# Optimization experiments

Measured on AMD Instinct MI355X. Metric: run time of the kernel, lower is better.

## Reference

```python
import jax, jax.numpy as jnp
import numpy as np

IN_C = 256
OUT_C = 256
HID = IN_C * 2
N_POINTS = 262144
N_NODES = 8192
B = 16
MAX_NODES = 512
EPS = 1e-5


def _mlp(h, w1, b1, g1, be1, w2, b2):
    # PyG MLP([C, 2C, out], norm='layer_norm'): lin -> layernorm -> relu -> (dropout, eval=identity) -> lin
    h = h @ w1 + b1
    mu = jnp.mean(h, axis=-1, keepdims=True)
    var = jnp.var(h, axis=-1, keepdims=True)
    h = (h - mu) * jax.lax.rsqrt(var + EPS) * g1 + be1
    h = jax.nn.relu(h)
    return h @ w2 + b2


def setup_inputs() -> dict:
    key = jax.random.key(0)
    ks = jax.random.split(key, 16)
    x = jax.random.normal(ks[0], (N_POINTS, IN_C), dtype=jnp.float32)
    f_point_batches = jnp.sort(jax.random.randint(ks[1], (N_POINTS,), 0, N_NODES)).astype(jnp.int32)
    # equal-sized graphs (16 graphs x 512 nodes), sorted as torch.split/pad_sequence assume
    g_node_batches = jnp.repeat(jnp.arange(B, dtype=jnp.int32), MAX_NODES)
    s = 1.0 / np.sqrt(IN_C)
    s2 = 1.0 / np.sqrt(HID)
    def lin(k, fan_in, shape, scale):
        return jax.random.uniform(k, shape, jnp.float32, -scale, scale)
    params = {}
    for i, name in enumerate(['Wq', 'Wk']):
        base = 2 + i * 6
        params[f'{name}_w1'] = lin(ks[base + 0], IN_C, (IN_C, HID), s)
        params[f'{name}_b1'] = lin(ks[base + 1], IN_C, (HID,), s)
        params[f'{name}_g1'] = jnp.ones((HID,), jnp.float32)
        params[f'{name}_be1'] = jnp.zeros((HID,), jnp.float32)
        params[f'{name}_w2'] = lin(ks[base + 2], HID, (HID, OUT_C), s2)
        params[f'{name}_b2'] = lin(ks[base + 3], HID, (OUT_C,), s2)
    return dict(x=x, f_point_batches=f_point_batches, g_node_batches=g_node_batches,
                num_graphs=B, max_nodes=MAX_NODES, **params)


def reference(x, f_point_batches, g_node_batches, num_graphs, max_nodes,
              Wq_w1, Wq_b1, Wq_g1, Wq_be1, Wq_w2, Wq_b2,
              Wk_w1, Wk_b1, Wk_g1, Wk_be1, Wk_w2, Wk_b2):
    n_nodes = g_node_batches.shape[0]
    C = x.shape[1]
    # scatter_mean over points -> per-node feature means [n_nodes, C]
    sums = jax.ops.segment_sum(x, f_point_batches, num_segments=n_nodes)
    cnt = jax.ops.segment_sum(jnp.ones((x.shape[0],), x.dtype), f_point_batches, num_segments=n_nodes)
    mean = sums / jnp.maximum(cnt, 1.0)[:, None]
    # ragged split by graph + pad_sequence -> [B, max_nodes, C]
    starts = jnp.searchsorted(g_node_batches, jnp.arange(num_graphs, dtype=g_node_batches.dtype))
    pos = jnp.arange(n_nodes) - starts[g_node_batches]
    padded = jnp.zeros((num_graphs, max_nodes, C), x.dtype).at[g_node_batches, pos].set(mean, mode='drop')
    q = _mlp(padded, Wq_w1, Wq_b1, Wq_g1, Wq_be1, Wq_w2, Wq_b2)  # [B, MAXN, out]
    k = _mlp(padded, Wk_w1, Wk_b1, Wk_g1, Wk_be1, Wk_w2, Wk_b2)
    return jnp.einsum('bnd,bmd->bnm', q, k)  # bmm(q, k^T)
```

## Files before the change

### kernel.cpp

```cpp
#include <hip/hip_runtime.h>
#include <hip/hip_bf16.h>

#define N_POINTS 262144
#define N_NODES  8192
#define IN_C     256
#define HID      512
#define OUT_C    256
#define NB       16
#define MAXN     512
#define EPSV     1e-5f
#define NPB      32

typedef __attribute__((ext_vector_type(8))) short short8;
typedef __attribute__((ext_vector_type(4))) float f32x4;
typedef __attribute__((ext_vector_type(4))) float f4v;
#define MFMA16(a, b, c) __builtin_amdgcn_mfma_f32_16x16x32_bf16((a), (b), (c), 0, 0, 0)


__global__ __launch_bounds__(256) void prelude_k(
    const int* __restrict__ fpb, int* __restrict__ starts,
    const float* __restrict__ W1q, const float* __restrict__ W1k,
    const float* __restrict__ W2q, const float* __restrict__ W2k,
    __hip_bfloat16* __restrict__ P1q, __hip_bfloat16* __restrict__ P1k,
    __hip_bfloat16* __restrict__ P2q, __hip_bfloat16* __restrict__ P2k)
{
  if (blockIdx.x < 1024) {
    const int i = blockIdx.x * 256 + threadIdx.x;
    const int cur = fpb[i];
    const int prev = (i == 0) ? -1 : fpb[i - 1];
    for (int n = prev + 1; n <= cur; ++n) starts[n] = i;
    if (i == N_POINTS - 1)
      for (int n = cur + 1; n <= N_NODES; ++n) starts[n] = N_POINTS;
    return;
  }
  const int bid = blockIdx.x - 1024;
  const int sel = bid >> 6;
  const float* W; __hip_bfloat16* P; int N;
  switch (sel) {
    case 0:  W = W1q; P = P1q; N = HID;   break;
    case 1:  W = W1k; P = P1k; N = HID;   break;
    case 2:  W = W2q; P = P2q; N = OUT_C; break;
    default: W = W2k; P = P2k; N = OUT_C; break;
  }
  const int idx = (bid & 63) * 256 + threadIdx.x;
  const int NF = N >> 4;
  const int lane = idx & 63;
  const int nf = (idx >> 6) % NF;
  const int ks = idx / (64 * NF);
  const int k0 = ks * 32 + (lane >> 4) * 8;
  const int n  = nf * 16 + (lane & 15);
  __hip_bfloat16 tmp[8];
  #pragma unroll
  for (int j = 0; j < 8; ++j) tmp[j] = __float2bfloat16(W[(size_t)(k0 + j) * N + n]);
  *(uint4*)(P + (size_t)idx * 8) = *(uint4*)tmp;
}

__device__ __forceinline__ void accum_rows(
    const float* __restrict__ x, int lo, int hi, int l,
    f4v& a0, f4v& a1, f4v& a2, f4v& a3)
{
  int r = lo;
  for (; r + 4 <= hi; r += 4) {
    f4v v0 = *(const f4v*)(x + (size_t)(r + 0) * IN_C + l * 4);
    f4v v1 = *(const f4v*)(x + (size_t)(r + 1) * IN_C + l * 4);
    f4v v2 = *(const f4v*)(x + (size_t)(r + 2) * IN_C + l * 4);
    f4v v3 = *(const f4v*)(x + (size_t)(r + 3) * IN_C + l * 4);
    a0 += v0; a1 += v1; a2 += v2; a3 += v3;
  }
  for (; r < hi; ++r)
    a0 += *(const f4v*)(x + (size_t)r * IN_C + l * 4);
}

__global__ __launch_bounds__(512, 4) void fused_mlp_k(
    const float* __restrict__ x, const int* __restrict__ starts,
    const __hip_bfloat16* __restrict__ P1q, const __hip_bfloat16* __restrict__ P2q,
    const float* __restrict__ b1q, const float* __restrict__ g1q,
    const float* __restrict__ be1q, const float* __restrict__ b2q,
    const __hip_bfloat16* __restrict__ P1k, const __hip_bfloat16* __restrict__ P2k,
    const float* __restrict__ b1k, const float* __restrict__ g1k,
    const float* __restrict__ be1k, const float* __restrict__ b2k,
    __hip_bfloat16* __restrict__ qo, __hip_bfloat16* __restrict__ ko)
{
  const int n0 = blockIdx.x * NPB;
  const int t = threadIdx.x;
  const int w = t >> 6, l = t & 63, lg = l >> 4, lm = l & 15;

  __shared__ __hip_bfloat16 As[NPB * 264];
  __shared__ __hip_bfloat16 Hs[NPB * 520];
  __shared__ float lnp[8][NPB][2];

  #pragma unroll
  for (int i = 0; i < 4; ++i) {
    const int nl = w * 4 + i;
    const int node = n0 + nl;
    const int s_ = starts[node], e_ = starts[node + 1];
    f4v a0 = (f4v)0.f, a1 = (f4v)0.f, a2 = (f4v)0.f, a3 = (f4v)0.f;
    accum_rows(x, s_, e_, l, a0, a1, a2, a3);
    a0 += a1 + a2 + a3;
    const int cnt = e_ - s_;
    const float inv = cnt > 0 ? 1.0f / (float)cnt : 0.0f;
    __hip_bfloat16 o[4];
    o[0] = __float2bfloat16(a0.x * inv);
    o[1] = __float2bfloat16(a0.y * inv);
    o[2] = __float2bfloat16(a0.z * inv);
    o[3] = __float2bfloat16(a0.w * inv);
    *(uint2*)(As + nl * 264 + l * 4) = *(uint2*)o;
  }
  __syncthreads();

  for (int hh = 0; hh < 2; ++hh) {
    const __hip_bfloat16* P1 = hh ? P1k : P1q;
    const __hip_bfloat16* P2 = hh ? P2k : P2q;
    const float* b1  = hh ? b1k  : b1q;
    const float* g1  = hh ? g1k  : g1q;
    const float* be1 = hh ? be1k : be1q;
    const float* b2  = hh ? b2k  : b2q;
    __hip_bfloat16* out = hh ? ko : qo;

    f32x4 acc1[2][4];
    #pragma unroll
    for (int mi = 0; mi < 2; ++mi)
      #pragma unroll
      for (int nj = 0; nj < 4; ++nj)
        #pragma unroll
        for (int r = 0; r < 4; ++r) acc1[mi][nj][r] = 0.f;

    for (int ks = 0; ks < 8; ++ks) {
      short8 a0 = *(const short8*)(As + lm * 264 + ks * 32 + lg * 8);
      short8 a1 = *(const short8*)(As + (16 + lm) * 264 + ks * 32 + lg * 8);
      const __hip_bfloat16* bp = P1 + ((size_t)(ks * 32 + w * 4) * 64 + l) * 8;
      #pragma unroll
      for (int nj = 0; nj < 4; ++nj) {
        short8 b = *(const short8*)(bp + (size_t)nj * 512);
        acc1[0][nj] = MFMA16(a0, b, acc1[0][nj]);
        acc1[1][nj] = MFMA16(a1, b, acc1[1][nj]);
      }
    }

    float b1v[4], g1v[4], e1v[4];
    #pragma unroll
    for (int nj = 0; nj < 4; ++nj) {
      const int col = w * 64 + nj * 16 + lm;
      b1v[nj] = b1[col]; g1v[nj] = g1[col]; e1v[nj] = be1[col];
    }
    #pragma unroll
    for (int mi = 0; mi < 2; ++mi)
      #pragma unroll
      for (int nj = 0; nj < 4; ++nj)
        #pragma unroll
        for (int r = 0; r < 4; ++r) acc1[mi][nj][r] += b1v[nj];

    #pragma unroll
    for (int mi = 0; mi < 2; ++mi)
      #pragma unroll
      for (int r = 0; r < 4; ++r) {
        float s = 0.f, q = 0.f;
        #pragma unroll
        for (int nj = 0; nj < 4; ++nj) {
          const float v = acc1[mi][nj][r];
          s += v; q += v * v;
        }
        #pragma unroll
        for (int off = 1; off < 16; off <<= 1) {
          s += __shfl_xor(s, off);
          q += __shfl_xor(q, off);
        }
        if (lm == 0) {
          const int row = mi * 16 + lg * 4 + r;
          lnp[w][row][0] = s;
          lnp[w][row][1] = q;
        }
      }
    __syncthreads();

    #pragma unroll
    for (int mi = 0; mi < 2; ++mi)
      #pragma unroll
      for (int r = 0; r < 4; ++r) {
        const int row = mi * 16 + lg * 4 + r;
        float S = 0.f, Q = 0.f;
        #pragma unroll
        for (int w2 = 0; w2 < 8; ++w2) {
          S += lnp[w2][row][0];
          Q += lnp[w2][row][1];
        }
        const float mu = S * (1.0f / HID);
        const float rs = rsqrtf(Q * (1.0f / HID) - mu * mu + EPSV);
        #pragma unroll
        for (int nj = 0; nj < 4; ++nj) {
          const float y = (acc1[mi][nj][r] - mu) * rs * g1v[nj] + e1v[nj];
          Hs[row * 520 + w * 64 + nj * 16 + lm] = __float2bfloat16(fmaxf(y, 0.f));
        }
      }
    __syncthreads();

    f32x4 acc2[2][2];
    #pragma unroll
    for (int mi = 0; mi < 2; ++mi)
      #pragma unroll
      for (int nj = 0; nj < 2; ++nj)
        #pragma unroll
        for (int r = 0; r < 4; ++r) acc2[mi][nj][r] = 0.f;

    for (int ks = 0; ks < 16; ++ks) {
      short8 a0 = *(const short8*)(Hs + lm * 520 + ks * 32 + lg * 8);
      short8 a1 = *(const short8*)(Hs + (16 + lm) * 520 + ks * 32 + lg * 8);
      const __hip_bfloat16* bp = P2 + ((size_t)(ks * 16 + w * 2) * 64 + l) * 8;
      #pragma unroll
      for (int nj = 0; nj < 2; ++nj) {
        short8 b = *(const short8*)(bp + (size_t)nj * 512);
        acc2[0][nj] = MFMA16(a0, b, acc2[0][nj]);
        acc2[1][nj] = MFMA16(a1, b, acc2[1][nj]);
      }
    }

    float b2v[2];
    #pragma unroll
    for (int nj = 0; nj < 2; ++nj) b2v[nj] = b2[w * 32 + nj * 16 + lm];
    #pragma unroll
    for (int mi = 0; mi < 2; ++mi)
      #pragma unroll
      for (int nj = 0; nj < 2; ++nj)
        #pragma unroll
        for (int r = 0; r < 4; ++r) {
          const int row = n0 + mi * 16 + lg * 4 + r;
          const int col = w * 32 + nj * 16 + lm;
          out[(size_t)row * OUT_C + col] = __float2bfloat16(acc2[mi][nj][r] + b2v[nj]);
        }
    __syncthreads();
  }
}

__global__ __launch_bounds__(256, 4) void bmm_k(
    const __hip_bfloat16* __restrict__ q, const __hip_bfloat16* __restrict__ k,
    float* __restrict__ out)
{
  const int b  = blockIdx.z;
  const int n0 = blockIdx.x * 64;
  const int m0 = blockIdx.y * 64;
  const int t = threadIdx.x;
  const int w = t >> 6, l = t & 63, lg = l >> 4, lm = l & 15;

  const __hip_bfloat16* qb = q + ((size_t)b * MAXN + n0 + w * 16) * OUT_C;
  const __hip_bfloat16* kb = k + ((size_t)b * MAXN + m0) * OUT_C;

  f32x4 acc[4];
  #pragma unroll
  for (int nj = 0; nj < 4; ++nj)
    #pragma unroll
    for (int r = 0; r < 4; ++r) acc[nj][r] = 0.f;

  for (int ks = 0; ks < 8; ++ks) {
    short8 a = *(const short8*)(qb + (size_t)lm * OUT_C + ks * 32 + lg * 8);
    #pragma unroll
    for (int nj = 0; nj < 4; ++nj) {
      short8 bb = *(const short8*)(kb + (size_t)(nj * 16 + lm) * OUT_C + ks * 32 + lg * 8);
      acc[nj] = MFMA16(a, bb, acc[nj]);
    }
  }

  #pragma unroll
  for (int nj = 0; nj < 4; ++nj)
    #pragma unroll
    for (int r = 0; r < 4; ++r) {
      const int nrow = n0 + w * 16 + lg * 4 + r;
      const int mcol = m0 + nj * 16 + lm;
      out[((size_t)b * MAXN + nrow) * MAXN + mcol] = acc[nj][r];
    }
}

extern "C" void kernel_launch(void* const* d_in, const int* in_sizes, int n_in,
                              void* d_out, int out_size, void* d_ws, size_t ws_size,
                              hipStream_t stream)
{
  const float* x   = (const float*)d_in[0];
  const int*   fpb = (const int*)d_in[1];
  const float* Wq_w1  = (const float*)d_in[5];
  const float* Wq_b1  = (const float*)d_in[6];
  const float* Wq_g1  = (const float*)d_in[7];
  const float* Wq_be1 = (const float*)d_in[8];
  const float* Wq_w2  = (const float*)d_in[9];
  const float* Wq_b2  = (const float*)d_in[10];
  const float* Wk_w1  = (const float*)d_in[11];
  const float* Wk_b1  = (const float*)d_in[12];
  const float* Wk_g1  = (const float*)d_in[13];
  const float* Wk_be1 = (const float*)d_in[14];
  const float* Wk_w2  = (const float*)d_in[15];
  const float* Wk_b2  = (const float*)d_in[16];

  __hip_bfloat16* ws = (__hip_bfloat16*)d_ws;
  __hip_bfloat16* P1q  = ws;
  __hip_bfloat16* P1k  = P1q + 131072;
  __hip_bfloat16* P2q  = P1k + 131072;
  __hip_bfloat16* P2k  = P2q + 131072;
  __hip_bfloat16* qo   = P2k + 131072;
  __hip_bfloat16* ko   = qo + 2097152;
  int* starts = (int*)(ko + 2097152);
  float* out = (float*)d_out;

  prelude_k<<<1280, 256, 0, stream>>>(fpb, starts,
      Wq_w1, Wk_w1, Wq_w2, Wk_w2, P1q, P1k, P2q, P2k);
  fused_mlp_k<<<N_NODES / NPB, 512, 0, stream>>>(
      x, starts, P1q, P2q, Wq_b1, Wq_g1, Wq_be1, Wq_b2,
      P1k, P2k, Wk_b1, Wk_g1, Wk_be1, Wk_b2, qo, ko);
  bmm_k<<<dim3(8, 8, NB), 256, 0, stream>>>(qo, ko, out);
}
```

Before: 96.19 us.

## Run Q and K MLP heads concurrently with 1024-thread blocks

The fused MLP kernel doubles its block to 16 waves. The first 8 waves compute the Q head and the other 8 compute the K head at the same time, instead of looping over the two heads one after the other. Each wave now gathers scatter-mean for 2 nodes instead of 4. The hidden buffer and the layernorm partials are duplicated per head, which raises LDS use and per-block register pressure. Launch bounds of 1024 threads with 4 blocks requested may not be achievable, so occupancy could drop.

```diff
diff --git a/kernel.cpp b/kernel.cpp
--- a/kernel.cpp
+++ b/kernel.cpp
@@ -71,7 +71,7 @@
     a0 += *(const f4v*)(x + (size_t)r * IN_C + l * 4);
 }
 
-__global__ __launch_bounds__(512, 4) void fused_mlp_k(
+__global__ __launch_bounds__(1024, 4) void fused_mlp_k(
     const float* __restrict__ x, const int* __restrict__ starts,
     const __hip_bfloat16* __restrict__ P1q, const __hip_bfloat16* __restrict__ P2q,
     const float* __restrict__ b1q, const float* __restrict__ g1q,
@@ -84,14 +84,25 @@
   const int n0 = blockIdx.x * NPB;
   const int t = threadIdx.x;
   const int w = t >> 6, l = t & 63, lg = l >> 4, lm = l & 15;
+  const int h = w >> 3;
+  const int c = w & 7;
+
+  const __hip_bfloat16* P1 = h ? P1k : P1q;
+  const __hip_bfloat16* P2 = h ? P2k : P2q;
+  const float* b1  = h ? b1k  : b1q;
+  const float* g1  = h ? g1k  : g1q;
+  const float* be1 = h ? be1k : be1q;
+  const float* b2  = h ? b2k  : b2q;
+  __hip_bfloat16* out = h ? ko : qo;
 
   __shared__ __hip_bfloat16 As[NPB * 264];
-  __shared__ __hip_bfloat16 Hs[NPB * 520];
-  __shared__ float lnp[8][NPB][2];
-
-  #pragma unroll
-  for (int i = 0; i < 4; ++i) {
-    const int nl = w * 4 + i;
+  __shared__ __hip_bfloat16 Hs[2][NPB * 520];
+  __shared__ float lnp[16][NPB][2];
+  __hip_bfloat16* Hsh = Hs[h];
+
+  #pragma unroll
+  for (int i = 0; i < 2; ++i) {
+    const int nl = w * 2 + i;
     const int node = n0 + nl;
     const int s_ = starts[node], e_ = starts[node + 1];
     f4v a0 = (f4v)0.f, a1 = (f4v)0.f, a2 = (f4v)0.f, a3 = (f4v)0.f;
@@ -108,127 +119,116 @@
   }
   __syncthreads();
 
-  for (int hh = 0; hh < 2; ++hh) {
-    const __hip_bfloat16* P1 = hh ? P1k : P1q;
-    const __hip_bfloat16* P2 = hh ? P2k : P2q;
-    const float* b1  = hh ? b1k  : b1q;
-    const float* g1  = hh ? g1k  : g1q;
-    const float* be1 = hh ? be1k : be1q;
-    const float* b2  = hh ? b2k  : b2q;
-    __hip_bfloat16* out = hh ? ko : qo;
-
-    f32x4 acc1[2][4];
-    #pragma unroll
-    for (int mi = 0; mi < 2; ++mi)
-      #pragma unroll
-      for (int nj = 0; nj < 4; ++nj)
-        #pragma unroll
-        for (int r = 0; r < 4; ++r) acc1[mi][nj][r] = 0.f;
-
-    for (int ks = 0; ks < 8; ++ks) {
-      short8 a0 = *(const short8*)(As + lm * 264 + ks * 32 + lg * 8);
-      short8 a1 = *(const short8*)(As + (16 + lm) * 264 + ks * 32 + lg * 8);
-      const __hip_bfloat16* bp = P1 + ((size_t)(ks * 32 + w * 4) * 64 + l) * 8;
+  f32x4 acc1[2][4];
+  #pragma unroll
+  for (int mi = 0; mi < 2; ++mi)
+    #pragma unroll
+    for (int nj = 0; nj < 4; ++nj)
+      #pragma unroll
+      for (int r = 0; r < 4; ++r) acc1[mi][nj][r] = 0.f;
+
+  for (int ks = 0; ks < 8; ++ks) {
+    short8 a0 = *(const short8*)(As + lm * 264 + ks * 32 + lg * 8);
+    short8 a1 = *(const short8*)(As + (16 + lm) * 264 + ks * 32 + lg * 8);
+    const __hip_bfloat16* bp = P1 + ((size_t)(ks * 32 + c * 4) * 64 + l) * 8;
+    #pragma unroll
+    for (int nj = 0; nj < 4; ++nj) {
+      short8 b = *(const short8*)(bp + (size_t)nj * 512);
+      acc1[0][nj] = MFMA16(a0, b, acc1[0][nj]);
+      acc1[1][nj] = MFMA16(a1, b, acc1[1][nj]);
+    }
+  }
+
+  float b1v[4], g1v[4], e1v[4];
+  #pragma unroll
+  for (int nj = 0; nj < 4; ++nj) {
+    const int col = c * 64 + nj * 16 + lm;
+    b1v[nj] = b1[col]; g1v[nj] = g1[col]; e1v[nj] = be1[col];
+  }
+  #pragma unroll
+  for (int mi = 0; mi < 2; ++mi)
+    #pragma unroll
+    for (int nj = 0; nj < 4; ++nj)
+      #pragma unroll
+      for (int r = 0; r < 4; ++r) acc1[mi][nj][r] += b1v[nj];
+
+  #pragma unroll
+  for (int mi = 0; mi < 2; ++mi)
+    #pragma unroll
+    for (int r = 0; r < 4; ++r) {
+      float s = 0.f, q = 0.f;
       #pragma unroll
       for (int nj = 0; nj < 4; ++nj) {
-        short8 b = *(const short8*)(bp + (size_t)nj * 512);
-        acc1[0][nj] = MFMA16(a0, b, acc1[0][nj]);
-        acc1[1][nj] = MFMA16(a1, b, acc1[1][nj]);
-      }
-    }
-
-    float b1v[4], g1v[4], e1v[4];
-    #pragma unroll
-    for (int nj = 0; nj < 4; ++nj) {
-      const int col = w * 64 + nj * 16 + lm;
-      b1v[nj] = b1[col]; g1v[nj] = g1[col]; e1v[nj] = be1[col];
-    }
-    #pragma unroll
-    for (int mi = 0; mi < 2; ++mi)
-      #pragma unroll
-      for (int nj = 0; nj < 4; ++nj)
-        #pragma unroll
-        for (int r = 0; r < 4; ++r) acc1[mi][nj][r] += b1v[nj];
-
-    #pragma unroll
-    for (int mi = 0; mi < 2; ++mi)
+        const float v = acc1[mi][nj][r];
+        s += v; q += v * v;
+      }
+      #pragma unroll
+      for (int off = 1; off < 16; off <<= 1) {
+        s += __shfl_xor(s, off);
+        q += __shfl_xor(q, off);
+      }
+      if (lm == 0) {
+        const int row = mi * 16 + lg * 4 + r;
+        lnp[w][row][0] = s;
+        lnp[w][row][1] = q;
+      }
+    }
+  __syncthreads();
+
+  #pragma unroll
+  for (int mi = 0; mi < 2; ++mi)
+    #pragma unroll
+    for (int r = 0; r < 4; ++r) {
+      const int row = mi * 16 + lg * 4 + r;
+      float S = 0.f, Q = 0.f;
+      #pragma unroll
+      for (int w2 = 0; w2 < 8; ++w2) {
+        S += lnp[h * 8 + w2][row][0];
+        Q += lnp[h * 8 + w2][row][1];
+      }
+      const float mu = S * (1.0f / HID);
+      const float rs = rsqrtf(Q * (1.0f / HID) - mu * mu + EPSV);
+      #pragma unroll
+      for (int nj = 0; nj < 4; ++nj) {
+        const float y = (acc1[mi][nj][r] - mu) * rs * g1v[nj] + e1v[nj];
+        Hsh[row * 520 + c * 64 + nj * 16 + lm] = __float2bfloat16(fmaxf(y, 0.f));
+      }
+    }
+  __syncthreads();
+
+  f32x4 acc2[2][2];
+  #pragma unroll
+  for (int mi = 0; mi < 2; ++mi)
+    #pragma unroll
+    for (int nj = 0; nj < 2; ++nj)
+      #pragma unroll
+      for (int r = 0; r < 4; ++r) acc2[mi][nj][r] = 0.f;
+
+  for (int ks = 0; ks < 16; ++ks) {
+    short8 a0 = *(const short8*)(Hsh + lm * 520 + ks * 32 + lg * 8);
+    short8 a1 = *(const short8*)(Hsh + (16 + lm) * 520 + ks * 32 + lg * 8);
+    const __hip_bfloat16* bp = P2 + ((size_t)(ks * 16 + c * 2) * 64 + l) * 8;
+    #pragma unroll
+    for (int nj = 0; nj < 2; ++nj) {
+      short8 b = *(const short8*)(bp + (size_t)nj * 512);
+      acc2[0][nj] = MFMA16(a0, b, acc2[0][nj]);
+      acc2[1][nj] = MFMA16(a1, b, acc2[1][nj]);
+    }
+  }
+
+  float b2v[2];
+  #pragma unroll
+  for (int nj = 0; nj < 2; ++nj) b2v[nj] = b2[c * 32 + nj * 16 + lm];
+  #pragma unroll
+  for (int mi = 0; mi < 2; ++mi)
+    #pragma unroll
+    for (int nj = 0; nj < 2; ++nj)
       #pragma unroll
       for (int r = 0; r < 4; ++r) {
-        float s = 0.f, q = 0.f;
-        #pragma unroll
-        for (int nj = 0; nj < 4; ++nj) {
-          const float v = acc1[mi][nj][r];
-          s += v; q += v * v;
-        }
-        #pragma unroll
-        for (int off = 1; off < 16; off <<= 1) {
-          s += __shfl_xor(s, off);
-          q += __shfl_xor(q, off);
-        }
-        if (lm == 0) {
-          const int row = mi * 16 + lg * 4 + r;
-          lnp[w][row][0] = s;
-          lnp[w][row][1] = q;
-        }
-      }
-    __syncthreads();
-
-    #pragma unroll
-    for (int mi = 0; mi < 2; ++mi)
-      #pragma unroll
-      for (int r = 0; r < 4; ++r) {
-        const int row = mi * 16 + lg * 4 + r;
-        float S = 0.f, Q = 0.f;
-        #pragma unroll
-        for (int w2 = 0; w2 < 8; ++w2) {
-          S += lnp[w2][row][0];
-          Q += lnp[w2][row][1];
-        }
-        const float mu = S * (1.0f / HID);
-        const float rs = rsqrtf(Q * (1.0f / HID) - mu * mu + EPSV);
-        #pragma unroll
-        for (int nj = 0; nj < 4; ++nj) {
-          const float y = (acc1[mi][nj][r] - mu) * rs * g1v[nj] + e1v[nj];
-          Hs[row * 520 + w * 64 + nj * 16 + lm] = __float2bfloat16(fmaxf(y, 0.f));
-        }
-      }
-    __syncthreads();
-
-    f32x4 acc2[2][2];
-    #pragma unroll
-    for (int mi = 0; mi < 2; ++mi)
-      #pragma unroll
-      for (int nj = 0; nj < 2; ++nj)
-        #pragma unroll
-        for (int r = 0; r < 4; ++r) acc2[mi][nj][r] = 0.f;
-
-    for (int ks = 0; ks < 16; ++ks) {
-      short8 a0 = *(const short8*)(Hs + lm * 520 + ks * 32 + lg * 8);
-      short8 a1 = *(const short8*)(Hs + (16 + lm) * 520 + ks * 32 + lg * 8);
-      const __hip_bfloat16* bp = P2 + ((size_t)(ks * 16 + w * 2) * 64 + l) * 8;
-      #pragma unroll
-      for (int nj = 0; nj < 2; ++nj) {
-        short8 b = *(const short8*)(bp + (size_t)nj * 512);
-        acc2[0][nj] = MFMA16(a0, b, acc2[0][nj]);
-        acc2[1][nj] = MFMA16(a1, b, acc2[1][nj]);
-      }
-    }
-
-    float b2v[2];
-    #pragma unroll
-    for (int nj = 0; nj < 2; ++nj) b2v[nj] = b2[w * 32 + nj * 16 + lm];
-    #pragma unroll
-    for (int mi = 0; mi < 2; ++mi)
-      #pragma unroll
-      for (int nj = 0; nj < 2; ++nj)
-        #pragma unroll
-        for (int r = 0; r < 4; ++r) {
-          const int row = n0 + mi * 16 + lg * 4 + r;
-          const int col = w * 32 + nj * 16 + lm;
-          out[(size_t)row * OUT_C + col] = __float2bfloat16(acc2[mi][nj][r] + b2v[nj]);
-        }
-    __syncthreads();
-  }
+        const int row = n0 + mi * 16 + lg * 4 + r;
+        const int col = c * 32 + nj * 16 + lm;
+        out[(size_t)row * OUT_C + col] = __float2bfloat16(acc2[mi][nj][r] + b2v[nj]);
+      }
 }
 
 __global__ __launch_bounds__(256, 4) void bmm_k(
@@ -300,7 +300,7 @@
 
   prelude_k<<<1280, 256, 0, stream>>>(fpb, starts,
       Wq_w1, Wk_w1, Wq_w2, Wk_w2, P1q, P1k, P2q, P2k);
-  fused_mlp_k<<<N_NODES / NPB, 512, 0, stream>>>(
+  fused_mlp_k<<<N_NODES / NPB, 1024, 0, stream>>>(
       x, starts, P1q, P2q, Wq_b1, Wq_g1, Wq_be1, Wq_b2,
       P1k, P2k, Wk_b1, Wk_g1, Wk_be1, Wk_b2, qo, ko);
   bmm_k<<<dim3(8, 8, NB), 256, 0, stream>>>(qo, ko, out);
```

After: 87.69 us. -8.8%, faster.
